# Optimization experiments

Measured on AMD Instinct MI355X. Metric: run time of the kernel, lower is better.

The kernel has to match this reference:

```python
import jax, jax.numpy as jnp
import numpy as np

EPS = 1e-12  # torch F.normalize eps


def _l2_normalize_dim1(v):
    # torch normalize(dim=1): normalize over the POINT/EDGE axis (quirk kept faithfully)
    n = jnp.sqrt(jnp.sum(v * v, axis=1, keepdims=True))
    return v / jnp.maximum(n, EPS)


def setup_inputs() -> dict:
    key = jax.random.key(0)
    k1, k2, k3, k4 = jax.random.split(key, 4)
    B, N, E = 4, 8192, 24576
    preds = jax.random.normal(k1, (B, N, 3), dtype=jnp.float32)
    gts = jax.random.normal(k2, (B, N, 3), dtype=jnp.float32)
    normals = jax.random.normal(k3, (B, N, 3), dtype=jnp.float32)
    edges = jax.random.randint(k4, (E, 2), 0, N, dtype=jnp.int32)
    return {"preds": preds, "gts": gts, "normals": normals, "edges": edges}


def reference(preds, gts, normals, edges):
    x, y = gts, preds  # P = batch_pairwise_dist(true, pred) -> [B, Nt, Np]
    xsq = jnp.sum(x * x, axis=-1)  # [B, Nt]
    ysq = jnp.sum(y * y, axis=-1)  # [B, Np]
    zz = jnp.einsum('bnd,bmd->bnm', x, y)  # [B, Nt, Np]
    P = xsq[:, :, None] + ysq[None if False else slice(None), None, :] - 2.0 * zz
    P = xsq[:, :, None] + ysq[:, None, :] - 2.0 * zz

    mins1 = jnp.min(P, axis=1)              # [B, Np] nearest true for each pred
    loss_1 = jnp.mean(mins1)
    mins2 = jnp.min(P, axis=2)              # [B, Nt] nearest pred for each true
    nearest_idx = jnp.argmin(P, axis=2)     # [B, Nt] indices into pred points
    loss_2 = jnp.mean(mins2)
    chamfer = loss_1 + loss_2

    e0 = edges[:, 0]
    e1 = edges[:, 1]
    edge_vectors = preds[:, e0, :] - preds[:, e1, :]           # [B, E, 3]
    edge_loss = jnp.mean(jnp.sum(edge_vectors * edge_vectors, axis=2))

    # gather normals at nearest-pred index per true point, then per edge start
    normals_nearest = jnp.take_along_axis(normals, nearest_idx[:, :, None], axis=1)  # [B, Nt, 3]
    normals_edge = normals_nearest[:, e0, :]                   # [B, E, 3]

    nn = _l2_normalize_dim1(normals_edge)
    nv = _l2_normalize_dim1(edge_vectors)
    cosines = jnp.abs(jnp.sum(nn * nv, axis=2))                # [B, E]
    normal_cosine_loss = jnp.mean(cosines)

    return 30000.0 * chamfer + 240.0 * edge_loss + 200000.0 * normal_cosine_loss
```

## Files before the change

kernel.cpp:

```cpp
#include <hip/hip_runtime.h>

namespace {

constexpr int B = 4;
constexpr int N = 8192;
constexpr int E = 24576;
constexpr int BN = B * N;
constexpr int BE = B * E;
constexpr int CHUNK = 256;
constexpr int RT = 4;

typedef float f32x2 __attribute__((ext_vector_type(2)));

__device__ __forceinline__ unsigned fkey(float f) {
  unsigned b = __float_as_uint(f);
  return b ^ ((b & 0x80000000u) ? 0xFFFFFFFFu : 0x80000000u);
}
__device__ __forceinline__ float funkey(unsigned k) {
  unsigned b = k ^ ((k & 0x80000000u) ? 0x80000000u : 0xFFFFFFFFu);
  return __uint_as_float(b);
}
__device__ __forceinline__ float min3f(float a, float b, float c) {
  float d;
  asm("v_min3_f32 %0, %1, %2, %3" : "=v"(d) : "v"(a), "v"(b), "v"(c));
  return d;
}
__device__ __forceinline__ f32x2 pk_fma_vsv(f32x2 a, f32x2 bs, f32x2 c) {
  f32x2 d;
  asm("v_pk_fma_f32 %0, %1, %2, %3" : "=v"(d) : "v"(a), "s"(bs), "v"(c));
  return d;
}
__device__ __forceinline__ f32x2 pk_fma_vvv(f32x2 a, f32x2 b, f32x2 c) {
  f32x2 d;
  asm("v_pk_fma_f32 %0, %1, %2, %3" : "=v"(d) : "v"(a), "v"(b), "v"(c));
  return d;
}


__global__ __launch_bounds__(256) void prep_kernel(const float* __restrict__ preds,
                                                   const float* __restrict__ gts,
                                                   float4* __restrict__ A,
                                                   float4* __restrict__ G,
                                                   float* __restrict__ A2f,
                                                   float* __restrict__ G2f,
                                                   unsigned long long* __restrict__ m2,
                                                   unsigned* __restrict__ m1,
                                                   float* __restrict__ sums) {
  int i = blockIdx.x * 256 + threadIdx.x;
  float px = preds[3*i], py = preds[3*i+1], pz = preds[3*i+2];
  float gx = gts[3*i],   gy = gts[3*i+1],  gz = gts[3*i+2];
  float ax = -2.f*px, ay = -2.f*py, az = -2.f*pz, aw = px*px + py*py + pz*pz;
  float bx = -2.f*gx, by = -2.f*gy, bz = -2.f*gz, bw = gx*gx + gy*gy + gz*gz;
  A[i] = make_float4(ax, ay, az, aw);
  G[i] = make_float4(bx, by, bz, bw);
  int p8 = (i >> 1) * 8, l = i & 1;
  A2f[p8 + 0 + l] = ax; A2f[p8 + 2 + l] = ay; A2f[p8 + 4 + l] = az; A2f[p8 + 6 + l] = aw;
  G2f[p8 + 0 + l] = bx; G2f[p8 + 2 + l] = by; G2f[p8 + 4 + l] = bz; G2f[p8 + 6 + l] = bw;
  m2[i] = ~0ULL;
  m1[i] = 0xFFFFFFFFu;
  if (i < 32) sums[i] = 0.f;
}

__global__ __launch_bounds__(256) void pass_wave(const float4* __restrict__ A,
                                                 const float4* __restrict__ G,
                                                 const float4* __restrict__ A2,
                                                 const float4* __restrict__ G2,
                                                 unsigned long long* __restrict__ m2,
                                                 unsigned* __restrict__ m1) {
  const int wid  = __builtin_amdgcn_readfirstlane((int)(threadIdx.x >> 6));
  const int lane = threadIdx.x & 63;
  const int u    = blockIdx.x * 4 + wid;
  const int ck = u & 31, rg = (u >> 5) & 31, b = (u >> 10) & 3, which = u >> 12;
  const float4* __restrict__ R  = which ? A  : G;
  const float4* __restrict__ S2 = which ? G2 : A2;
  const float4* __restrict__ Sg = S2 + b * N + ck * CHUNK;
  const int base = ck * CHUNK;
  f32x2 x2[RT], y2[RT], z2[RT];
  float w[RT], best[RT];
#pragma unroll
  for (int i = 0; i < RT; ++i) {
    float4 r = R[b * N + rg * (64 * RT) + i * 64 + lane];
    float xx = -0.5f * r.x, yy = -0.5f * r.y, zz = -0.5f * r.z;
    x2[i] = f32x2{xx, xx}; y2[i] = f32x2{yy, yy}; z2[i] = f32x2{zz, zz};
    w[i] = r.w; best[i] = 3.4e38f;
  }
  if (which == 0) {
    int wjj[RT];
#pragma unroll
    for (int i = 0; i < RT; ++i) wjj[i] = 0;
#pragma unroll 8
    for (int jr = 0; jr < CHUNK / 2; ++jr) {
      float4 qa = Sg[2*jr], qb = Sg[2*jr + 1];
      f32x2 qx = f32x2{qa.x, qa.y}, qy = f32x2{qa.z, qa.w};
      f32x2 qz = f32x2{qb.x, qb.y}, qw = f32x2{qb.z, qb.w};
#pragma unroll
      for (int i = 0; i < RT; ++i) {
        f32x2 t = pk_fma_vsv(z2[i], qz, qw);
        t = pk_fma_vsv(y2[i], qy, t);
        t = pk_fma_vsv(x2[i], qx, t);
        float m = min3f(best[i], t.x, t.y);
        wjj[i] = (m < best[i]) ? 2*jr : wjj[i];
        best[i] = m;
      }
    }
#pragma unroll
    for (int i = 0; i < RT; ++i) {
      float4 qa = Sg[wjj[i]], qb = Sg[wjj[i] + 1];
      f32x2 t = pk_fma_vvv(z2[i], f32x2{qb.x, qb.y}, f32x2{qb.z, qb.w});
      t = pk_fma_vvv(y2[i], f32x2{qa.z, qa.w}, t);
      t = pk_fma_vvv(x2[i], f32x2{qa.x, qa.y}, t);
      const int idx = base + wjj[i] + ((t.x <= t.y) ? 0 : 1);
      const int gi = b * N + rg * (64 * RT) + i * 64 + lane;
      float d = w[i] + best[i];
      atomicMin(&m2[gi], ((unsigned long long)fkey(d) << 32) | (unsigned)idx);
    }
  } else {
#pragma unroll 8
    for (int jr = 0; jr < CHUNK / 2; ++jr) {
      float4 qa = Sg[2*jr], qb = Sg[2*jr + 1];
      f32x2 qx = f32x2{qa.x, qa.y}, qy = f32x2{qa.z, qa.w};
      f32x2 qz = f32x2{qb.x, qb.y}, qw = f32x2{qb.z, qb.w};
#pragma unroll
      for (int i = 0; i < RT; ++i) {
        f32x2 t = pk_fma_vsv(z2[i], qz, qw);
        t = pk_fma_vsv(y2[i], qy, t);
        t = pk_fma_vsv(x2[i], qx, t);
        best[i] = min3f(best[i], t.x, t.y);
      }
    }
#pragma unroll
    for (int i = 0; i < RT; ++i) {
      const int gi = b * N + rg * (64 * RT) + i * 64 + lane;
      atomicMin(&m1[gi], fkey(w[i] + best[i]));
    }
  }
}

__global__ __launch_bounds__(256) void edgeA_kernel(const float* __restrict__ preds,
                                                    const float* __restrict__ normals,
                                                    const int* __restrict__ edges,
                                                    const unsigned long long* __restrict__ m2,
                                                    const unsigned* __restrict__ m1,
                                                    float* __restrict__ ev,
                                                    float* __restrict__ sums) {
  __shared__ float ws[4][6];
  const int tid = threadIdx.x;
  const int wid = tid >> 6, lane = tid & 63;
  if (blockIdx.x < 384) {
    const int b = blockIdx.x / 96;
    const int e = (blockIdx.x % 96) * 256 + tid;
    int e0 = edges[2*e], e1 = edges[2*e+1];
    const float* pb = preds   + 3*(size_t)b*N;
    const float* nb = normals + 3*(size_t)b*N;
    float vx = pb[3*e0]   - pb[3*e1];
    float vy = pb[3*e0+1] - pb[3*e1+1];
    float vz = pb[3*e0+2] - pb[3*e1+2];
    unsigned ni = (unsigned)m2[b*N + e0];
    float nx = nb[3*ni], ny = nb[3*ni+1], nz = nb[3*ni+2];
    const int be = b * E + e;
    ev[0*BE + be] = vx; ev[1*BE + be] = vy; ev[2*BE + be] = vz;
    ev[3*BE + be] = nx; ev[4*BE + be] = ny; ev[5*BE + be] = nz;
    float v[6] = {nx*nx, ny*ny, nz*nz, vx*vx, vy*vy, vz*vz};
#pragma unroll
    for (int k = 0; k < 6; ++k)
#pragma unroll
      for (int o = 32; o; o >>= 1) v[k] += __shfl_down(v[k], o, 64);
    if (lane == 0) {
#pragma unroll
      for (int k = 0; k < 6; ++k) ws[wid][k] = v[k];
    }
    __syncthreads();
    if (tid < 6) {
      const int k = tid;
      float t = ws[0][k] + ws[1][k] + ws[2][k] + ws[3][k];
      atomicAdd(&sums[(k < 3 ? 3 + k : 12 + k) + b*3], t);
    }
  } else {
    int i = (blockIdx.x - 384) * 256 + tid;
    float d2 = funkey((unsigned)(m2[i] >> 32));
    float d1 = funkey(m1[i]);
#pragma unroll
    for (int o = 32; o; o >>= 1) { d2 += __shfl_down(d2, o, 64); d1 += __shfl_down(d1, o, 64); }
    if (lane == 0) { ws[wid][0] = d2; ws[wid][1] = d1; }
    __syncthreads();
    if (tid == 0) {
      atomicAdd(&sums[1], ws[0][0] + ws[1][0] + ws[2][0] + ws[3][0]);
      atomicAdd(&sums[0], ws[0][1] + ws[1][1] + ws[2][1] + ws[3][1]);
    }
  }
}

__global__ __launch_bounds__(256) void edgeB_kernel(const float* __restrict__ ev,
                                                    float* __restrict__ sums,
                                                    float* __restrict__ out) {
  __shared__ float ws[4];
  __shared__ bool amLast;
  const int tid = threadIdx.x;
  const int b = blockIdx.x / 96;
  const int e = (blockIdx.x % 96) * 256 + tid;
  const int be = b * E + e;
  float vx = ev[0*BE + be], vy = ev[1*BE + be], vz = ev[2*BE + be];
  float nx = ev[3*BE + be], ny = ev[4*BE + be], nz = ev[5*BE + be];
  float inn0 = 1.f / fmaxf(sqrtf(sums[3  + b*3 + 0]), 1e-12f);
  float inn1 = 1.f / fmaxf(sqrtf(sums[3  + b*3 + 1]), 1e-12f);
  float inn2 = 1.f / fmaxf(sqrtf(sums[3  + b*3 + 2]), 1e-12f);
  float inv0 = 1.f / fmaxf(sqrtf(sums[15 + b*3 + 0]), 1e-12f);
  float inv1 = 1.f / fmaxf(sqrtf(sums[15 + b*3 + 1]), 1e-12f);
  float inv2 = 1.f / fmaxf(sqrtf(sums[15 + b*3 + 2]), 1e-12f);
  float c = fabsf(nx*inn0*vx*inv0 + ny*inn1*vy*inv1 + nz*inn2*vz*inv2);
#pragma unroll
  for (int o = 32; o; o >>= 1) c += __shfl_down(c, o, 64);
  if ((tid & 63) == 0) ws[tid >> 6] = c;
  __syncthreads();
  if (tid == 0) {
    atomicAdd(&sums[2], ws[0] + ws[1] + ws[2] + ws[3]);
    __threadfence();
    unsigned old = atomicAdd((unsigned*)(sums + 30), 1u);
    amLast = (old == 383u);
  }
  __syncthreads();
  if (amLast && tid == 0) {
    float esum = 0.f;
#pragma unroll
    for (int i = 0; i < 12; ++i) esum += atomicAdd(&sums[15 + i], 0.f);
    float s0 = atomicAdd(&sums[0], 0.f), s1 = atomicAdd(&sums[1], 0.f);
    float s2 = atomicAdd(&sums[2], 0.f);
    float chamfer   = (s0 + s1) * (1.f / (float)BN);
    float edge_loss = esum * (1.f / (float)(B * E));
    float ncl       = s2 * (1.f / (float)(B * E));
    out[0] = 30000.f * chamfer + 240.f * edge_loss + 200000.f * ncl;
  }
}

}

extern "C" void kernel_launch(void* const* d_in, const int* in_sizes, int n_in,
                              void* d_out, int out_size, void* d_ws, size_t ws_size,
                              hipStream_t stream) {
  (void)in_sizes; (void)n_in; (void)out_size; (void)ws_size;
  const float* preds   = (const float*)d_in[0];
  const float* gts     = (const float*)d_in[1];
  const float* normals = (const float*)d_in[2];
  const int*   edges   = (const int*)d_in[3];
  char* ws = (char*)d_ws;
  float4*             A    = (float4*)(ws);
  float4*             G    = (float4*)(ws + 0x080000);
  float4*             A2   = (float4*)(ws + 0x100000);
  float4*             G2   = (float4*)(ws + 0x180000);
  unsigned long long* m2   = (unsigned long long*)(ws + 0x200000);
  unsigned*           m1   = (unsigned*)(ws + 0x240000);
  float*              sums = (float*)(ws + 0x260000);
  float*              ev   = (float*)(ws + 0x261000);
  float* out = (float*)d_out;

  prep_kernel<<<dim3(BN/256), 256, 0, stream>>>(preds, gts, A, G, (float*)A2, (float*)G2,
                                                m2, m1, sums);
  pass_wave<<<dim3(2048), 256, 0, stream>>>(A, G, A2, G2, m2, m1);
  edgeA_kernel<<<dim3(512), 256, 0, stream>>>(preds, normals, edges, m2, m1, ev, sums);
  edgeB_kernel<<<dim3(384), 256, 0, stream>>>(ev, sums, out);
}
```

Baseline: 78.42 us.

## Replace brute-force nearest-neighbour search with uniform-grid spatial binning

The all-pairs distance pass is replaced by a 32^3 uniform grid per batch and point set. New kernels count points per cell, prefix-scan the counts, scatter points into cell order, and search outward in growing cubic rings, stopping once the best distance is inside the ring radius. Ties are broken by original index to keep argmin semantics. This removes the quadratic distance work, at the cost of several extra kernel launches, atomics and divergent ring loops for sparse tail points. The fixed grid bounds assume coordinates roughly within ±4.2, and points outside are clamped into border cells.

```diff
diff --git a/kernel.cpp b/kernel.cpp
--- a/kernel.cpp
+++ b/kernel.cpp
@@ -7,10 +7,11 @@
 constexpr int E = 24576;
 constexpr int BN = B * N;
 constexpr int BE = B * E;
-constexpr int CHUNK = 256;
-constexpr int RT = 4;
-
-typedef float f32x2 __attribute__((ext_vector_type(2)));
+constexpr int GS = 32;
+constexpr int NC = GS * GS * GS;
+constexpr float LO = -4.2f;
+constexpr float CS = 0.2625f;
+constexpr float INV = 1.0f / 0.2625f;
 
 __device__ __forceinline__ unsigned fkey(float f) {
   unsigned b = __float_as_uint(f);
@@ -20,119 +21,142 @@
   unsigned b = k ^ ((k & 0x80000000u) ? 0x80000000u : 0xFFFFFFFFu);
   return __uint_as_float(b);
 }
-__device__ __forceinline__ float min3f(float a, float b, float c) {
-  float d;
-  asm("v_min3_f32 %0, %1, %2, %3" : "=v"(d) : "v"(a), "v"(b), "v"(c));
-  return d;
-}
-__device__ __forceinline__ f32x2 pk_fma_vsv(f32x2 a, f32x2 bs, f32x2 c) {
-  f32x2 d;
-  asm("v_pk_fma_f32 %0, %1, %2, %3" : "=v"(d) : "v"(a), "s"(bs), "v"(c));
-  return d;
-}
-__device__ __forceinline__ f32x2 pk_fma_vvv(f32x2 a, f32x2 b, f32x2 c) {
-  f32x2 d;
-  asm("v_pk_fma_f32 %0, %1, %2, %3" : "=v"(d) : "v"(a), "v"(b), "v"(c));
-  return d;
-}
-
-
-__global__ __launch_bounds__(256) void prep_kernel(const float* __restrict__ preds,
-                                                   const float* __restrict__ gts,
-                                                   float4* __restrict__ A,
-                                                   float4* __restrict__ G,
-                                                   float* __restrict__ A2f,
-                                                   float* __restrict__ G2f,
-                                                   unsigned long long* __restrict__ m2,
-                                                   unsigned* __restrict__ m1,
-                                                   float* __restrict__ sums) {
+__device__ __forceinline__ int clamp31(int v) { return v < 0 ? 0 : (v > 31 ? 31 : v); }
+
+
+__global__ __launch_bounds__(256) void z0_kernel(uint4* __restrict__ cnt4,
+                                                 float* __restrict__ sums) {
   int i = blockIdx.x * 256 + threadIdx.x;
+  cnt4[i] = uint4{0u, 0u, 0u, 0u};
+  if (i < 32) sums[i] = 0.f;
+}
+
+__global__ __launch_bounds__(256) void prep2_kernel(const float* __restrict__ preds,
+                                                    const float* __restrict__ gts,
+                                                    float4* __restrict__ A,
+                                                    float4* __restrict__ G,
+                                                    unsigned* __restrict__ cellA,
+                                                    unsigned* __restrict__ cellG,
+                                                    unsigned* __restrict__ cnt) {
+  int i = blockIdx.x * 256 + threadIdx.x;
+  int b = i >> 13;
   float px = preds[3*i], py = preds[3*i+1], pz = preds[3*i+2];
   float gx = gts[3*i],   gy = gts[3*i+1],  gz = gts[3*i+2];
-  float ax = -2.f*px, ay = -2.f*py, az = -2.f*pz, aw = px*px + py*py + pz*pz;
-  float bx = -2.f*gx, by = -2.f*gy, bz = -2.f*gz, bw = gx*gx + gy*gy + gz*gz;
-  A[i] = make_float4(ax, ay, az, aw);
-  G[i] = make_float4(bx, by, bz, bw);
-  int p8 = (i >> 1) * 8, l = i & 1;
-  A2f[p8 + 0 + l] = ax; A2f[p8 + 2 + l] = ay; A2f[p8 + 4 + l] = az; A2f[p8 + 6 + l] = aw;
-  G2f[p8 + 0 + l] = bx; G2f[p8 + 2 + l] = by; G2f[p8 + 4 + l] = bz; G2f[p8 + 6 + l] = bw;
-  m2[i] = ~0ULL;
-  m1[i] = 0xFFFFFFFFu;
-  if (i < 32) sums[i] = 0.f;
-}
-
-__global__ __launch_bounds__(256) void pass_wave(const float4* __restrict__ A,
-                                                 const float4* __restrict__ G,
-                                                 const float4* __restrict__ A2,
-                                                 const float4* __restrict__ G2,
-                                                 unsigned long long* __restrict__ m2,
-                                                 unsigned* __restrict__ m1) {
-  const int wid  = __builtin_amdgcn_readfirstlane((int)(threadIdx.x >> 6));
-  const int lane = threadIdx.x & 63;
-  const int u    = blockIdx.x * 4 + wid;
-  const int ck = u & 31, rg = (u >> 5) & 31, b = (u >> 10) & 3, which = u >> 12;
-  const float4* __restrict__ R  = which ? A  : G;
-  const float4* __restrict__ S2 = which ? G2 : A2;
-  const float4* __restrict__ Sg = S2 + b * N + ck * CHUNK;
-  const int base = ck * CHUNK;
-  f32x2 x2[RT], y2[RT], z2[RT];
-  float w[RT], best[RT];
-#pragma unroll
-  for (int i = 0; i < RT; ++i) {
-    float4 r = R[b * N + rg * (64 * RT) + i * 64 + lane];
-    float xx = -0.5f * r.x, yy = -0.5f * r.y, zz = -0.5f * r.z;
-    x2[i] = f32x2{xx, xx}; y2[i] = f32x2{yy, yy}; z2[i] = f32x2{zz, zz};
-    w[i] = r.w; best[i] = 3.4e38f;
-  }
-  if (which == 0) {
-    int wjj[RT];
-#pragma unroll
-    for (int i = 0; i < RT; ++i) wjj[i] = 0;
-#pragma unroll 8
-    for (int jr = 0; jr < CHUNK / 2; ++jr) {
-      float4 qa = Sg[2*jr], qb = Sg[2*jr + 1];
-      f32x2 qx = f32x2{qa.x, qa.y}, qy = f32x2{qa.z, qa.w};
-      f32x2 qz = f32x2{qb.x, qb.y}, qw = f32x2{qb.z, qb.w};
-#pragma unroll
-      for (int i = 0; i < RT; ++i) {
-        f32x2 t = pk_fma_vsv(z2[i], qz, qw);
-        t = pk_fma_vsv(y2[i], qy, t);
-        t = pk_fma_vsv(x2[i], qx, t);
-        float m = min3f(best[i], t.x, t.y);
-        wjj[i] = (m < best[i]) ? 2*jr : wjj[i];
-        best[i] = m;
+  A[i] = make_float4(-2.f*px, -2.f*py, -2.f*pz, px*px + py*py + pz*pz);
+  G[i] = make_float4(-2.f*gx, -2.f*gy, -2.f*gz, gx*gx + gy*gy + gz*gz);
+  int ax = clamp31((int)floorf((px - LO) * INV));
+  int ay = clamp31((int)floorf((py - LO) * INV));
+  int az = clamp31((int)floorf((pz - LO) * INV));
+  unsigned ca = (unsigned)((az << 10) | (ay << 5) | ax);
+  int bx_ = clamp31((int)floorf((gx - LO) * INV));
+  int by_ = clamp31((int)floorf((gy - LO) * INV));
+  int bz_ = clamp31((int)floorf((gz - LO) * INV));
+  unsigned cg = (unsigned)((bz_ << 10) | (by_ << 5) | bx_);
+  cellA[i] = ca; cellG[i] = cg;
+  atomicAdd(&cnt[((unsigned)(0*4 + b) << 15) + ca], 1u);
+  atomicAdd(&cnt[((unsigned)(1*4 + b) << 15) + cg], 1u);
+}
+
+__global__ __launch_bounds__(1024) void scan_kernel(const unsigned* __restrict__ cnt,
+                                                    unsigned* __restrict__ offs,
+                                                    unsigned* __restrict__ fill) {
+  __shared__ unsigned sd[1024];
+  const unsigned base = (unsigned)blockIdx.x << 15;
+  const int t = threadIdx.x;
+  const unsigned cbase = base + (unsigned)t * 32u;
+  unsigned s = 0;
+  for (int j = 0; j < 32; ++j) s += cnt[cbase + j];
+  sd[t] = s;
+  __syncthreads();
+  for (int off = 1; off < 1024; off <<= 1) {
+    unsigned v = (t >= off) ? sd[t - off] : 0u;
+    __syncthreads();
+    sd[t] += v;
+    __syncthreads();
+  }
+  unsigned run = (t == 0) ? 0u : sd[t - 1];
+  for (int j = 0; j < 32; ++j) {
+    unsigned c = cnt[cbase + j];
+    offs[cbase + j] = run;
+    fill[cbase + j] = run;
+    run += c;
+  }
+}
+
+__global__ __launch_bounds__(256) void scatter_kernel(const float4* __restrict__ A,
+                                                      const float4* __restrict__ G,
+                                                      const unsigned* __restrict__ cellA,
+                                                      const unsigned* __restrict__ cellG,
+                                                      unsigned* __restrict__ fill,
+                                                      float4* __restrict__ sA,
+                                                      unsigned* __restrict__ iA,
+                                                      float4* __restrict__ sG,
+                                                      unsigned* __restrict__ iG) {
+  int i = blockIdx.x * 256 + threadIdx.x;
+  int b = i >> 13;
+  unsigned n = (unsigned)(i & (N - 1));
+  unsigned ca = cellA[i];
+  unsigned slot = atomicAdd(&fill[((unsigned)(0*4 + b) << 15) + ca], 1u);
+  sA[(b << 13) + slot] = A[i]; iA[(b << 13) + slot] = n;
+  unsigned cg = cellG[i];
+  slot = atomicAdd(&fill[((unsigned)(1*4 + b) << 15) + cg], 1u);
+  sG[(b << 13) + slot] = G[i]; iG[(b << 13) + slot] = n;
+}
+
+__global__ __launch_bounds__(256) void query_kernel(const float4* __restrict__ sA,
+                                                    const unsigned* __restrict__ iA,
+                                                    const float4* __restrict__ sG,
+                                                    const unsigned* __restrict__ iG,
+                                                    const unsigned* __restrict__ offs,
+                                                    const unsigned* __restrict__ cnt,
+                                                    unsigned long long* __restrict__ m2,
+                                                    unsigned* __restrict__ m1) {
+  const int t = blockIdx.x * 256 + threadIdx.x;
+  const int sub = t & 3;
+  const int p = t >> 2;
+  const int which = p >> 15;
+  const int q = p & 32767;
+  const int b = q >> 13, j = q & 8191;
+  const float4* __restrict__ sq   = which ? sA : sG;
+  const unsigned* __restrict__ sqi = which ? iA : iG;
+  const float4* __restrict__ db   = which ? sG : sA;
+  const unsigned* __restrict__ dbi = which ? iG : iA;
+  const unsigned gb = ((unsigned)((which << 2) + b)) << 15;
+  float4 qr = sq[(b << 13) + j];
+  unsigned orig = sqi[(b << 13) + j];
+  const float px = -0.5f * qr.x, py = -0.5f * qr.y, pz = -0.5f * qr.z, w = qr.w;
+  const int cx = clamp31((int)floorf((px - LO) * INV));
+  const int cy = clamp31((int)floorf((py - LO) * INV));
+  const int cz = clamp31((int)floorf((pz - LO) * INV));
+  const float4* __restrict__ dbb = db + (b << 13);
+  const unsigned* __restrict__ dbib = dbi + (b << 13);
+  unsigned long long best = ~0ULL;
+  for (int R = 1; R <= 32; ++R) {
+    const int x0 = cx - R < 0 ? 0 : cx - R, x1 = cx + R > 31 ? 31 : cx + R;
+    const int y0 = cy - R < 0 ? 0 : cy - R, y1 = cy + R > 31 ? 31 : cy + R;
+    const int z0 = cz - R < 0 ? 0 : cz - R, z1 = cz + R > 31 ? 31 : cz + R;
+    for (int zz = z0; zz <= z1; ++zz) {
+      for (int yy = y0; yy <= y1; ++yy) {
+        const unsigned rowb = gb + (unsigned)((zz << 10) | (yy << 5));
+        const int s = (int)offs[rowb + x0];
+        const int e = (int)(offs[rowb + x1] + cnt[rowb + x1]);
+        for (int k = s + sub; k < e; k += 4) {
+          float4 c = dbb[k];
+          float d = w + fmaf(px, c.x, fmaf(py, c.y, fmaf(pz, c.z, c.w)));
+          unsigned long long key = ((unsigned long long)fkey(d) << 32) | dbib[k];
+          best = key < best ? key : best;
+        }
       }
     }
-#pragma unroll
-    for (int i = 0; i < RT; ++i) {
-      float4 qa = Sg[wjj[i]], qb = Sg[wjj[i] + 1];
-      f32x2 t = pk_fma_vvv(z2[i], f32x2{qb.x, qb.y}, f32x2{qb.z, qb.w});
-      t = pk_fma_vvv(y2[i], f32x2{qa.z, qa.w}, t);
-      t = pk_fma_vvv(x2[i], f32x2{qa.x, qa.y}, t);
-      const int idx = base + wjj[i] + ((t.x <= t.y) ? 0 : 1);
-      const int gi = b * N + rg * (64 * RT) + i * 64 + lane;
-      float d = w[i] + best[i];
-      atomicMin(&m2[gi], ((unsigned long long)fkey(d) << 32) | (unsigned)idx);
-    }
-  } else {
-#pragma unroll 8
-    for (int jr = 0; jr < CHUNK / 2; ++jr) {
-      float4 qa = Sg[2*jr], qb = Sg[2*jr + 1];
-      f32x2 qx = f32x2{qa.x, qa.y}, qy = f32x2{qa.z, qa.w};
-      f32x2 qz = f32x2{qb.x, qb.y}, qw = f32x2{qb.z, qb.w};
-#pragma unroll
-      for (int i = 0; i < RT; ++i) {
-        f32x2 t = pk_fma_vsv(z2[i], qz, qw);
-        t = pk_fma_vsv(y2[i], qy, t);
-        t = pk_fma_vsv(x2[i], qx, t);
-        best[i] = min3f(best[i], t.x, t.y);
-      }
-    }
-#pragma unroll
-    for (int i = 0; i < RT; ++i) {
-      const int gi = b * N + rg * (64 * RT) + i * 64 + lane;
-      atomicMin(&m1[gi], fkey(w[i] + best[i]));
-    }
+    unsigned long long o = __shfl_xor(best, 1, 64); best = o < best ? o : best;
+    o = __shfl_xor(best, 2, 64); best = o < best ? o : best;
+    float bd = funkey((unsigned)(best >> 32));
+    float rr = (float)R * CS;
+    if (bd <= rr * rr) break;
+  }
+  if (sub == 0) {
+    if (which == 0) m2[(b << 13) + orig] = best;
+    else            m1[(b << 13) + orig] = (unsigned)(best >> 32);
   }
 }
 
@@ -172,8 +196,8 @@
     __syncthreads();
     if (tid < 6) {
       const int k = tid;
-      float t = ws[0][k] + ws[1][k] + ws[2][k] + ws[3][k];
-      atomicAdd(&sums[(k < 3 ? 3 + k : 12 + k) + b*3], t);
+      float s = ws[0][k] + ws[1][k] + ws[2][k] + ws[3][k];
+      atomicAdd(&sums[(k < 3 ? 3 + k : 12 + k) + b*3], s);
     }
   } else {
     int i = (blockIdx.x - 384) * 256 + tid;
@@ -243,19 +267,28 @@
   const float* normals = (const float*)d_in[2];
   const int*   edges   = (const int*)d_in[3];
   char* ws = (char*)d_ws;
-  float4*             A    = (float4*)(ws);
-  float4*             G    = (float4*)(ws + 0x080000);
-  float4*             A2   = (float4*)(ws + 0x100000);
-  float4*             G2   = (float4*)(ws + 0x180000);
-  unsigned long long* m2   = (unsigned long long*)(ws + 0x200000);
-  unsigned*           m1   = (unsigned*)(ws + 0x240000);
-  float*              sums = (float*)(ws + 0x260000);
-  float*              ev   = (float*)(ws + 0x261000);
+  float4*             A     = (float4*)(ws);
+  float4*             G     = (float4*)(ws + 0x080000);
+  unsigned*           cellA = (unsigned*)(ws + 0x100000);
+  unsigned*           cellG = (unsigned*)(ws + 0x120000);
+  unsigned*           cnt   = (unsigned*)(ws + 0x140000);
+  unsigned*           offs  = (unsigned*)(ws + 0x240000);
+  unsigned*           fill  = (unsigned*)(ws + 0x340000);
+  float4*             sA    = (float4*)(ws + 0x440000);
+  float4*             sG    = (float4*)(ws + 0x4C0000);
+  unsigned*           iA    = (unsigned*)(ws + 0x540000);
+  unsigned*           iG    = (unsigned*)(ws + 0x560000);
+  unsigned long long* m2    = (unsigned long long*)(ws + 0x580000);
+  unsigned*           m1    = (unsigned*)(ws + 0x5C0000);
+  float*              sums  = (float*)(ws + 0x5E0000);
+  float*              ev    = (float*)(ws + 0x140000);
   float* out = (float*)d_out;
 
-  prep_kernel<<<dim3(BN/256), 256, 0, stream>>>(preds, gts, A, G, (float*)A2, (float*)G2,
-                                                m2, m1, sums);
-  pass_wave<<<dim3(2048), 256, 0, stream>>>(A, G, A2, G2, m2, m1);
+  z0_kernel<<<dim3(256), 256, 0, stream>>>((uint4*)cnt, sums);
+  prep2_kernel<<<dim3(BN/256), 256, 0, stream>>>(preds, gts, A, G, cellA, cellG, cnt);
+  scan_kernel<<<dim3(8), 1024, 0, stream>>>(cnt, offs, fill);
+  scatter_kernel<<<dim3(BN/256), 256, 0, stream>>>(A, G, cellA, cellG, fill, sA, iA, sG, iG);
+  query_kernel<<<dim3(1024), 256, 0, stream>>>(sA, iA, sG, iG, offs, cnt, m2, m1);
   edgeA_kernel<<<dim3(512), 256, 0, stream>>>(preds, normals, edges, m2, m1, ev, sums);
   edgeB_kernel<<<dim3(384), 256, 0, stream>>>(ev, sums, out);
 }
```

After: 266.7 us. 240% more time.
